# Kernel optimization log

Hardware: AMD Instinct MI355X
Metric: run time of the kernel (lower is better)

Reference implementation:

```python
import jax, jax.numpy as jnp
import numpy as np

K_PERIODS = 4
PMAX = 64
MIN_PERIOD = 8


def setup_inputs() -> dict:
    key = jax.random.key(0)
    x = jax.random.normal(key, (32, 512, 64), dtype=jnp.float32)  # [B, T, N]
    return {"x": x}


def reference(x):
    """Dense, fixed-shape equivalent of PeriodicityTransform.forward (mask=None).

    Instead of a Python list of variable-shape PeriodGroup tiles, returns a
    padded tensor values[bn, k, c, p] where for each (sequence bn, freq rank k)
    with period P and cycles C, values[bn, k, :C, :P] equals the torch tile
    seqs[bn, T-C*P : T].reshape(C, P); entries outside (C, P) are zero.
    Also returns the integer periods and cycles per (bn, k).
    """
    B, T, N = x.shape
    BN = B * N
    seqs = jnp.transpose(x, (0, 2, 1)).reshape(BN, T)  # [BN, T]

    # top-k nonzero FFT frequencies (DC bin zeroed out)
    spec = jnp.fft.rfft(seqs, axis=-1)
    mag2 = spec.real ** 2 + spec.imag ** 2
    mag2 = mag2.at[..., 0].set(0.0)
    _, kidx = jax.lax.top_k(mag2, K_PERIODS)  # [BN, K]
    kidx = jnp.maximum(kidx, 1)

    # periods = clamp(T // f, min=MIN_PERIOD, max=PMAX); cycles = T // period
    periods = jnp.clip(T // kidx, MIN_PERIOD, PMAX)  # [BN, K]
    cycles = T // periods                              # [BN, K]

    cmax = T // MIN_PERIOD  # static upper bound on cycles
    i = jnp.arange(cmax)[:, None]   # cycle index  [Cmax, 1]
    j = jnp.arange(PMAX)[None, :]   # phase index  [1, Pmax]

    start = T - cycles * periods                                   # [BN, K]
    idx = start[..., None, None] + i * periods[..., None, None] + j  # [BN,K,Cmax,Pmax]
    idx = jnp.clip(idx, 0, T - 1)
    valid = (i < cycles[..., None, None]) & (j < periods[..., None, None])

    gathered = jnp.take_along_axis(
        seqs[:, None, :], idx.reshape(BN, K_PERIODS, -1), axis=-1
    ).reshape(BN, K_PERIODS, cmax, PMAX)
    values = jnp.where(valid, gathered, jnp.float32(0.0))
    return values, periods, cycles
```

## Files before the change

### kernel.cpp

```cpp
#include <hip/hip_runtime.h>
#include <math.h>

#define TT 512
#define KP 4

typedef unsigned long long u64;

#define SYNCL() asm volatile("s_waitcnt lgkmcnt(0)\n\ts_barrier" ::: "memory")

__global__ __launch_bounds__(256) void periodicity_kernel(const float* __restrict__ x,
                                                          float* __restrict__ out) {
    const int bn   = blockIdx.x;
    const int tid  = threadIdx.x;
    const int lane = tid & 63;
    const int wid  = tid >> 6;
    const int b = bn >> 6;
    const int n = bn & 63;

    __shared__ float2 tw[TT];
    __shared__ __align__(16) float row[TT];
    __shared__ float2 buf[TT];
    __shared__ u64    keys[256];
    __shared__ int    fin8[8];
    __shared__ float  candMagF[8];
    __shared__ double candV8[8];
    __shared__ unsigned char w4tab[64];

    float sv, cv;
    sincosf((float)(2.0 * M_PI / 512.0) * (float)tid, &sv, &cv);
    tw[tid]       = make_float2(cv, -sv);
    tw[tid + 256] = make_float2(-cv, sv);
    if (tid < 64) {
        int W = 512 / (tid + 1);
        W = W < 8 ? 8 : (W > 64 ? 64 : W);
        w4tab[tid] = (unsigned char)((W + 3) >> 2);
    }

    const float* xb = x + (size_t)b * (TT * 64) + n;
    {
        float v0 = xb[(size_t)tid * 64];
        float v1 = xb[(size_t)(tid + 256) * 64];
        row[tid] = v0;  row[tid + 256] = v1;
        float sum = v0 + v1, dif = v0 - v1;
        buf[tid]       = make_float2(sum, 0.f);
        buf[tid + 256] = make_float2(dif * cv, -dif * sv);
    }
    SYNCL();

    float* outv = out + (size_t)bn * (KP * 64 * 64);
    {
        const int j  = tid & 15;
        const int cb = tid >> 4;
        #pragma unroll
        for (int iter = 0; iter < 4; ++iter) {
            const int c = 8 + iter * 16 + cb;
            if (c < 64 && j >= (int)w4tab[c]) {
                const float4 z = make_float4(0.f, 0.f, 0.f, 0.f);
                #pragma unroll
                for (int k = 0; k < KP; ++k)
                    *(float4*)(outv + k * 4096 + c * 64 + j * 4) = z;
            }
        }
    }

    #pragma unroll
    for (int stg = 0; stg < 4; ++stg) {
        if (tid < 128) {
            const int Q  = 64 >> (2 * stg);
            const int B4 = Q << 2;
            const int h  = tid >> 6;
            const int fj = tid & 63;
            const int g  = fj >> (6 - 2 * stg);
            const int i  = fj & (Q - 1);
            float2* bb = &buf[h << 8];
            const int base = g * B4 + i;
            float2 x0 = bb[base],         x1 = bb[base + Q];
            float2 x2 = bb[base + 2 * Q], x3 = bb[base + 3 * Q];
            float2 A  = make_float2(x0.x + x2.x, x0.y + x2.y);
            float2 Bm = make_float2(x0.x - x2.x, x0.y - x2.y);
            float2 Cc = make_float2(x1.x + x3.x, x1.y + x3.y);
            float2 D  = make_float2(x1.x - x3.x, x1.y - x3.y);
            float2 y0 = make_float2(A.x + Cc.x, A.y + Cc.y);
            float2 y2 = make_float2(A.x - Cc.x, A.y - Cc.y);
            float2 y1 = make_float2(Bm.x + D.y, Bm.y - D.x);
            float2 y3 = make_float2(Bm.x - D.y, Bm.y + D.x);
            const int m = i << (1 + 2 * stg);
            float2 t1 = tw[m], t2 = tw[2 * m], t3 = tw[3 * m];
            bb[base]         = y0;
            bb[base + Q]     = make_float2(y1.x * t1.x - y1.y * t1.y, y1.x * t1.y + y1.y * t1.x);
            bb[base + 2 * Q] = make_float2(y2.x * t2.x - y2.y * t2.y, y2.x * t2.y + y2.y * t2.x);
            bb[base + 3 * Q] = make_float2(y3.x * t3.x - y3.y * t3.y, y3.x * t3.y + y3.y * t3.x);
        }
        SYNCL();
    }

    #pragma unroll
    for (int hh = 0; hh < 2; ++hh) {
        const int p = tid;
        const int kp = ((p & 3) << 6) | (((p >> 2) & 3) << 4) | (((p >> 4) & 3) << 2) | ((p >> 6) & 3);
        const int f = 2 * kp + hh;
        if (f >= 1 && f <= 256) {
            float2 v = buf[hh * 256 + p];
            float mag = v.x * v.x + v.y * v.y;
            keys[f - 1] = ((u64)__float_as_uint(mag) << 32) | (u64)(255 - (f - 1));
        }
    }
    SYNCL();

    if (wid == 0) {
        u64 k0 = keys[lane * 4 + 0];
        u64 k1 = keys[lane * 4 + 1];
        u64 k2 = keys[lane * 4 + 2];
        u64 k3 = keys[lane * 4 + 3];
        #define CSWAP(a, b) { if (a < b) { u64 _t = a; a = b; b = _t; } }
        CSWAP(k0, k1) CSWAP(k2, k3) CSWAP(k0, k2) CSWAP(k1, k3) CSWAP(k1, k2)
        #undef CSWAP
        #pragma unroll
        for (int r = 0; r < 8; ++r) {
            u64 w = k0;
            #pragma unroll
            for (int off = 32; off >= 1; off >>= 1) {
                u64 o = __shfl_xor(w, off);
                if (o > w) w = o;
            }
            if (k0 == w) { k0 = k1; k1 = k2; k2 = k3; k3 = 0; }
            if (lane == 0) {
                fin8[r] = 256 - (int)(w & 0xff);
                candMagF[r] = __uint_as_float((unsigned)(w >> 32));
            }
        }
    }
    SYNCL();

    int per[KP], cycv[KP], stv[KP];
    {
        const float m0 = candMagF[0], m1 = candMagF[1], m2 = candMagF[2],
                    m3 = candMagF[3], m4 = candMagF[4];
        const bool needRefine = ((m0 - m1) <= 1e-4f * m0) || ((m1 - m2) <= 1e-4f * m1) ||
                                ((m2 - m3) <= 1e-4f * m2) || ((m3 - m4) <= 1e-4f * m3);
        int bins[KP];
        if (!needRefine) {
            #pragma unroll
            for (int k = 0; k < KP; ++k) bins[k] = fin8[k];
        } else {
            {
                const int cid = tid >> 5;
                const int sub = tid & 31;
                const int fc  = fin8[cid];
                const int t0  = sub * 16;
                const double W = 6.2831853071795864769 / 512.0;
                double zr, zi, wr, wi;
                sincos(W * (double)((fc * t0) & 511), &zi, &zr);
                sincos(W * (double)fc, &wi, &wr);
                double ar = 0.0, ai = 0.0;
                const float4* r4 = (const float4*)row;
                #pragma unroll
                for (int v4i = 0; v4i < 4; ++v4i) {
                    float4 xv = r4[sub * 4 + v4i];
                    #define STEP(comp)                                   \
                        { double xd = (double)xv.comp;                   \
                          ar = fma(xd, zr, ar); ai = fma(xd, zi, ai);    \
                          double tq = zr * wr - zi * wi;                 \
                          zi = fma(zr, wi, zi * wr); zr = tq; }
                    STEP(x) STEP(y) STEP(z) STEP(w)
                    #undef STEP
                }
                #pragma unroll
                for (int off = 16; off >= 1; off >>= 1) {
                    ar += __shfl_xor(ar, off);
                    ai += __shfl_xor(ai, off);
                }
                if (sub == 0) candV8[cid] = ar * ar + ai * ai;
            }
            SYNCL();
            unsigned chosen = 0;
            #pragma unroll
            for (int k = 0; k < KP; ++k) {
                double bv = -1.0; int bbin = 0x7fffffff; int bj = 0;
                #pragma unroll
                for (int j = 0; j < 8; ++j) {
                    if (chosen & (1u << j)) continue;
                    double vj = candV8[j];
                    int    bjn = fin8[j];
                    if (vj > bv || (vj == bv && bjn < bbin)) { bv = vj; bbin = bjn; bj = j; }
                }
                chosen |= (1u << bj);
                bins[k] = bbin;
            }
        }
        #pragma unroll
        for (int k = 0; k < KP; ++k) {
            int p = TT / bins[k];
            p = p < 8 ? 8 : (p > 64 ? 64 : p);
            per[k]  = p;
            cycv[k] = TT / p;
            stv[k]  = TT - cycv[k] * p;
        }
    }

    const size_t VOFF = (size_t)2048 * KP * 64 * 64;
    if (tid == 0) {
        #pragma unroll
        for (int k = 0; k < KP; ++k) {
            out[VOFF + (size_t)bn * KP + k]        = (float)per[k];
            out[VOFF + 8192 + (size_t)bn * KP + k] = (float)cycv[k];
        }
    }

    {
        const int c  = tid >> 2;
        const int j0 = tid & 3;
        const int W4c = (int)w4tab[c];
        #pragma unroll
        for (int k = 0; k < KP; ++k) {
            const int P = per[k], C = cycv[k], S0 = stv[k];
            const int inC  = (c < C) ? 1 : 0;
            const int base = S0 + c * P;
            #pragma unroll
            for (int m = 0; m < 4; ++m) {
                const int j = j0 + (m << 2);
                if (j < W4c) {
                    const int p0 = j << 2;
                    float4 v = make_float4(0.f, 0.f, 0.f, 0.f);
                    if (inC) {
                        if (p0     < P) v.x = row[base + p0];
                        if (p0 + 1 < P) v.y = row[base + p0 + 1];
                        if (p0 + 2 < P) v.z = row[base + p0 + 2];
                        if (p0 + 3 < P) v.w = row[base + p0 + 3];
                    }
                    *(float4*)(outv + k * 4096 + c * 64 + p0) = v;
                }
            }
        }
    }
}

extern "C" void kernel_launch(void* const* d_in, const int* in_sizes, int n_in,
                              void* d_out, int out_size, void* d_ws, size_t ws_size,
                              hipStream_t stream) {
    const float* x = (const float*)d_in[0];
    float* out = (float*)d_out;
    hipLaunchKernelGGL(periodicity_kernel, dim3(2048), dim3(256), 0, stream, x, out);
}
```

Baseline: 35.75 us.

## Process four sequences per block with warp-specialized FFT and store waves

Each block now handles four sequences: four waves each run a full radix-4 FFT, top-k selection and optional refinement for one sequence without block barriers, while four other waves zero-fill the padding and then write the gathered tiles once periods are published through shared memory. This removes most block-wide barriers from the FFT and sort stages and overlaps the zero-fill stores with the compute. It costs more shared memory per block and gives each FFT wave more serial work, since only 64 lanes now do each FFT. The grid shrinks to 512 blocks of 512 threads.

```diff
diff --git a/kernel.cpp b/kernel.cpp
--- a/kernel.cpp
+++ b/kernel.cpp
@@ -8,155 +8,147 @@
 
 #define SYNCL() asm volatile("s_waitcnt lgkmcnt(0)\n\ts_barrier" ::: "memory")
 
-__global__ __launch_bounds__(256) void periodicity_kernel(const float* __restrict__ x,
-                                                          float* __restrict__ out) {
-    const int bn   = blockIdx.x;
+__global__ __launch_bounds__(512, 4) void periodicity_kernel(const float* __restrict__ x,
+                                                             float* __restrict__ out) {
+    const int blk  = blockIdx.x;
     const int tid  = threadIdx.x;
     const int lane = tid & 63;
     const int wid  = tid >> 6;
-    const int b = bn >> 6;
-    const int n = bn & 63;
 
     __shared__ float2 tw[TT];
-    __shared__ __align__(16) float row[TT];
-    __shared__ float2 buf[TT];
-    __shared__ u64    keys[256];
-    __shared__ int    fin8[8];
-    __shared__ float  candMagF[8];
-    __shared__ double candV8[8];
-    __shared__ unsigned char w4tab[64];
-
-    float sv, cv;
-    sincosf((float)(2.0 * M_PI / 512.0) * (float)tid, &sv, &cv);
-    tw[tid]       = make_float2(cv, -sv);
-    tw[tid + 256] = make_float2(-cv, sv);
-    if (tid < 64) {
-        int W = 512 / (tid + 1);
-        W = W < 8 ? 8 : (W > 64 ? 64 : W);
-        w4tab[tid] = (unsigned char)((W + 3) >> 2);
+    __shared__ __align__(16) float rowl[4][TT];
+    __shared__ float2 buf[4][TT];
+    __shared__ u64    keys[4][256];
+    __shared__ int    fin8s[4][8];
+    __shared__ double candV8[4][8];
+    __shared__ int    pstore[4][12];
+
+    const size_t VOFF = (size_t)2048 * KP * 64 * 64;
+
+    float v[8];
+    if (wid < 4) {
+        const int bn = blk * 4 + wid;
+        const int b = bn >> 6, n = bn & 63;
+        const float* xb = x + (size_t)b * (TT * 64) + n;
+        #pragma unroll
+        for (int q = 0; q < 8; ++q) v[q] = xb[(size_t)(lane + 64 * q) * 64];
     }
 
-    const float* xb = x + (size_t)b * (TT * 64) + n;
     {
-        float v0 = xb[(size_t)tid * 64];
-        float v1 = xb[(size_t)(tid + 256) * 64];
-        row[tid] = v0;  row[tid + 256] = v1;
-        float sum = v0 + v1, dif = v0 - v1;
-        buf[tid]       = make_float2(sum, 0.f);
-        buf[tid + 256] = make_float2(dif * cv, -dif * sv);
+        float s, c;
+        sincosf((float)(2.0 * M_PI / 512.0) * (float)tid, &s, &c);
+        tw[tid] = make_float2(c, -s);
     }
     SYNCL();
 
-    float* outv = out + (size_t)bn * (KP * 64 * 64);
-    {
-        const int j  = tid & 15;
-        const int cb = tid >> 4;
-        #pragma unroll
-        for (int iter = 0; iter < 4; ++iter) {
-            const int c = 8 + iter * 16 + cb;
-            if (c < 64 && j >= (int)w4tab[c]) {
-                const float4 z = make_float4(0.f, 0.f, 0.f, 0.f);
-                #pragma unroll
-                for (int k = 0; k < KP; ++k)
-                    *(float4*)(outv + k * 4096 + c * 64 + j * 4) = z;
-            }
-        }
-    }
-
-    #pragma unroll
-    for (int stg = 0; stg < 4; ++stg) {
-        if (tid < 128) {
-            const int Q  = 64 >> (2 * stg);
-            const int B4 = Q << 2;
-            const int h  = tid >> 6;
-            const int fj = tid & 63;
-            const int g  = fj >> (6 - 2 * stg);
-            const int i  = fj & (Q - 1);
-            float2* bb = &buf[h << 8];
-            const int base = g * B4 + i;
-            float2 x0 = bb[base],         x1 = bb[base + Q];
-            float2 x2 = bb[base + 2 * Q], x3 = bb[base + 3 * Q];
-            float2 A  = make_float2(x0.x + x2.x, x0.y + x2.y);
-            float2 Bm = make_float2(x0.x - x2.x, x0.y - x2.y);
-            float2 Cc = make_float2(x1.x + x3.x, x1.y + x3.y);
-            float2 D  = make_float2(x1.x - x3.x, x1.y - x3.y);
-            float2 y0 = make_float2(A.x + Cc.x, A.y + Cc.y);
-            float2 y2 = make_float2(A.x - Cc.x, A.y - Cc.y);
-            float2 y1 = make_float2(Bm.x + D.y, Bm.y - D.x);
-            float2 y3 = make_float2(Bm.x - D.y, Bm.y + D.x);
-            const int m = i << (1 + 2 * stg);
-            float2 t1 = tw[m], t2 = tw[2 * m], t3 = tw[3 * m];
-            bb[base]         = y0;
-            bb[base + Q]     = make_float2(y1.x * t1.x - y1.y * t1.y, y1.x * t1.y + y1.y * t1.x);
-            bb[base + 2 * Q] = make_float2(y2.x * t2.x - y2.y * t2.y, y2.x * t2.y + y2.y * t2.x);
-            bb[base + 3 * Q] = make_float2(y3.x * t3.x - y3.y * t3.y, y3.x * t3.y + y3.y * t3.x);
-        }
-        SYNCL();
-    }
-
-    #pragma unroll
-    for (int hh = 0; hh < 2; ++hh) {
-        const int p = tid;
-        const int kp = ((p & 3) << 6) | (((p >> 2) & 3) << 4) | (((p >> 4) & 3) << 2) | ((p >> 6) & 3);
-        const int f = 2 * kp + hh;
-        if (f >= 1 && f <= 256) {
-            float2 v = buf[hh * 256 + p];
-            float mag = v.x * v.x + v.y * v.y;
-            keys[f - 1] = ((u64)__float_as_uint(mag) << 32) | (u64)(255 - (f - 1));
-        }
-    }
-    SYNCL();
-
-    if (wid == 0) {
-        u64 k0 = keys[lane * 4 + 0];
-        u64 k1 = keys[lane * 4 + 1];
-        u64 k2 = keys[lane * 4 + 2];
-        u64 k3 = keys[lane * 4 + 3];
-        #define CSWAP(a, b) { if (a < b) { u64 _t = a; a = b; b = _t; } }
-        CSWAP(k0, k1) CSWAP(k2, k3) CSWAP(k0, k2) CSWAP(k1, k3) CSWAP(k1, k2)
-        #undef CSWAP
-        #pragma unroll
-        for (int r = 0; r < 8; ++r) {
-            u64 w = k0;
-            #pragma unroll
-            for (int off = 32; off >= 1; off >>= 1) {
-                u64 o = __shfl_xor(w, off);
-                if (o > w) w = o;
-            }
-            if (k0 == w) { k0 = k1; k1 = k2; k2 = k3; k3 = 0; }
-            if (lane == 0) {
-                fin8[r] = 256 - (int)(w & 0xff);
-                candMagF[r] = __uint_as_float((unsigned)(w >> 32));
-            }
-        }
-    }
-    SYNCL();
-
-    int per[KP], cycv[KP], stv[KP];
-    {
-        const float m0 = candMagF[0], m1 = candMagF[1], m2 = candMagF[2],
-                    m3 = candMagF[3], m4 = candMagF[4];
-        const bool needRefine = ((m0 - m1) <= 1e-4f * m0) || ((m1 - m2) <= 1e-4f * m1) ||
-                                ((m2 - m3) <= 1e-4f * m2) || ((m3 - m4) <= 1e-4f * m3);
+    if (wid < 4) {
+        const int r  = wid;
+        const int bn = blk * 4 + r;
+
+        #pragma unroll
+        for (int q = 0; q < 8; ++q) rowl[r][lane + 64 * q] = v[q];
+        #pragma unroll
+        for (int q = 0; q < 4; ++q) {
+            const int t = lane + 64 * q;
+            float sum = v[q] + v[q + 4], dif = v[q] - v[q + 4];
+            float2 w = tw[t];
+            buf[r][t]       = make_float2(sum, 0.f);
+            buf[r][t + 256] = make_float2(dif * w.x, dif * w.y);
+        }
+
+        #pragma unroll
+        for (int stg = 0; stg < 4; ++stg) {
+            #pragma unroll
+            for (int h = 0; h < 2; ++h) {
+                const int Q  = 64 >> (2 * stg);
+                const int B4 = Q << 2;
+                const int g  = lane >> (6 - 2 * stg);
+                const int i  = lane & (Q - 1);
+                float2* bb = &buf[r][h << 8];
+                const int base = g * B4 + i;
+                float2 x0 = bb[base],         x1 = bb[base + Q];
+                float2 x2 = bb[base + 2 * Q], x3 = bb[base + 3 * Q];
+                float2 A  = make_float2(x0.x + x2.x, x0.y + x2.y);
+                float2 Bm = make_float2(x0.x - x2.x, x0.y - x2.y);
+                float2 Cc = make_float2(x1.x + x3.x, x1.y + x3.y);
+                float2 D  = make_float2(x1.x - x3.x, x1.y - x3.y);
+                float2 y0 = make_float2(A.x + Cc.x, A.y + Cc.y);
+                float2 y2 = make_float2(A.x - Cc.x, A.y - Cc.y);
+                float2 y1 = make_float2(Bm.x + D.y, Bm.y - D.x);
+                float2 y3 = make_float2(Bm.x - D.y, Bm.y + D.x);
+                const int m = i << (1 + 2 * stg);
+                float2 t1 = tw[m], t2 = tw[2 * m], t3 = tw[3 * m];
+                bb[base]         = y0;
+                bb[base + Q]     = make_float2(y1.x * t1.x - y1.y * t1.y, y1.x * t1.y + y1.y * t1.x);
+                bb[base + 2 * Q] = make_float2(y2.x * t2.x - y2.y * t2.y, y2.x * t2.y + y2.y * t2.x);
+                bb[base + 3 * Q] = make_float2(y3.x * t3.x - y3.y * t3.y, y3.x * t3.y + y3.y * t3.x);
+            }
+        }
+
+        #pragma unroll
+        for (int q = 0; q < 8; ++q) {
+            const int pos = lane + 64 * q;
+            const int p = pos & 255, h = pos >> 8;
+            const int kp = ((p & 3) << 6) | (((p >> 2) & 3) << 4) | (((p >> 4) & 3) << 2) | ((p >> 6) & 3);
+            const int f = 2 * kp + h;
+            if (f >= 1 && f <= 256) {
+                float2 vv = buf[r][pos];
+                float mag = vv.x * vv.x + vv.y * vv.y;
+                keys[r][f - 1] = ((u64)__float_as_uint(mag) << 32) | (u64)(255 - (f - 1));
+            }
+        }
+
+        int   fbin[8];
+        float cmag[8];
+        {
+            u64 k0 = keys[r][lane * 4 + 0];
+            u64 k1 = keys[r][lane * 4 + 1];
+            u64 k2 = keys[r][lane * 4 + 2];
+            u64 k3 = keys[r][lane * 4 + 3];
+            #define CSWAP(a, b) { if (a < b) { u64 _t = a; a = b; b = _t; } }
+            CSWAP(k0, k1) CSWAP(k2, k3) CSWAP(k0, k2) CSWAP(k1, k3) CSWAP(k1, k2)
+            #undef CSWAP
+            #pragma unroll
+            for (int rr = 0; rr < 8; ++rr) {
+                u64 w = k0;
+                #pragma unroll
+                for (int off = 32; off >= 1; off >>= 1) {
+                    u64 o = __shfl_xor(w, off);
+                    if (o > w) w = o;
+                }
+                if (k0 == w) { k0 = k1; k1 = k2; k2 = k3; k3 = 0; }
+                fbin[rr] = 256 - (int)(w & 0xff);
+                cmag[rr] = __uint_as_float((unsigned)(w >> 32));
+            }
+        }
+        if (lane == 0) {
+            #pragma unroll
+            for (int rr = 0; rr < 8; ++rr) fin8s[r][rr] = fbin[rr];
+        }
+
+        const bool needRefine =
+            ((cmag[0] - cmag[1]) <= 1e-4f * cmag[0]) || ((cmag[1] - cmag[2]) <= 1e-4f * cmag[1]) ||
+            ((cmag[2] - cmag[3]) <= 1e-4f * cmag[2]) || ((cmag[3] - cmag[4]) <= 1e-4f * cmag[3]);
+
         int bins[KP];
         if (!needRefine) {
             #pragma unroll
-            for (int k = 0; k < KP; ++k) bins[k] = fin8[k];
+            for (int k = 0; k < KP; ++k) bins[k] = fbin[k];
         } else {
             {
-                const int cid = tid >> 5;
-                const int sub = tid & 31;
-                const int fc  = fin8[cid];
-                const int t0  = sub * 16;
+                const int cid = lane >> 3;
+                const int sub = lane & 7;
+                const int fc  = fin8s[r][cid];
+                const int t0  = sub * 64;
                 const double W = 6.2831853071795864769 / 512.0;
                 double zr, zi, wr, wi;
                 sincos(W * (double)((fc * t0) & 511), &zi, &zr);
                 sincos(W * (double)fc, &wi, &wr);
                 double ar = 0.0, ai = 0.0;
-                const float4* r4 = (const float4*)row;
-                #pragma unroll
-                for (int v4i = 0; v4i < 4; ++v4i) {
-                    float4 xv = r4[sub * 4 + v4i];
+                const float4* r4 = (const float4*)rowl[r];
+                #pragma unroll
+                for (int v4i = 0; v4i < 16; ++v4i) {
+                    float4 xv = r4[sub * 16 + v4i];
                     #define STEP(comp)                                   \
                         { double xd = (double)xv.comp;                   \
                           ar = fma(xd, zr, ar); ai = fma(xd, zi, ai);    \
@@ -166,13 +158,12 @@
                     #undef STEP
                 }
                 #pragma unroll
-                for (int off = 16; off >= 1; off >>= 1) {
+                for (int off = 4; off >= 1; off >>= 1) {
                     ar += __shfl_xor(ar, off);
                     ai += __shfl_xor(ai, off);
                 }
-                if (sub == 0) candV8[cid] = ar * ar + ai * ai;
-            }
-            SYNCL();
+                if (sub == 0) candV8[r][cid] = ar * ar + ai * ai;
+            }
             unsigned chosen = 0;
             #pragma unroll
             for (int k = 0; k < KP; ++k) {
@@ -180,14 +171,16 @@
                 #pragma unroll
                 for (int j = 0; j < 8; ++j) {
                     if (chosen & (1u << j)) continue;
-                    double vj = candV8[j];
-                    int    bjn = fin8[j];
+                    double vj = candV8[r][j];
+                    int    bjn = fbin[j];
                     if (vj > bv || (vj == bv && bjn < bbin)) { bv = vj; bbin = bjn; bj = j; }
                 }
                 chosen |= (1u << bj);
                 bins[k] = bbin;
             }
         }
+
+        int per[KP], cycv[KP], stv[KP];
         #pragma unroll
         for (int k = 0; k < KP; ++k) {
             int p = TT / bins[k];
@@ -196,39 +189,72 @@
             cycv[k] = TT / p;
             stv[k]  = TT - cycv[k] * p;
         }
-    }
-
-    const size_t VOFF = (size_t)2048 * KP * 64 * 64;
-    if (tid == 0) {
+        if (lane == 0) {
+            #pragma unroll
+            for (int k = 0; k < KP; ++k) {
+                pstore[r][k]     = per[k];
+                pstore[r][4 + k] = cycv[k];
+                pstore[r][8 + k] = stv[k];
+                out[VOFF + (size_t)bn * KP + k]        = (float)per[k];
+                out[VOFF + 8192 + (size_t)bn * KP + k] = (float)cycv[k];
+            }
+        }
+        SYNCL();
+    } else {
+        const int r  = wid - 4;
+        const int bn = blk * 4 + r;
+        float* outv = out + (size_t)bn * (KP * 64 * 64);
+        const int cr = lane >> 4;
+        const int j  = lane & 15;
+        const float4 z = make_float4(0.f, 0.f, 0.f, 0.f);
+
+        #pragma unroll
+        for (int c0 = 8; c0 < 64; c0 += 4) {
+            const int c = c0 + cr;
+            int W = 512 / (c + 1);
+            W = W < 8 ? 8 : W;
+            const int W4c = (W + 3) >> 2;
+            if (j >= W4c) {
+                #pragma unroll
+                for (int k = 0; k < KP; ++k)
+                    *(float4*)(outv + k * 4096 + c * 64 + j * 4) = z;
+            }
+        }
+        SYNCL();
+
+        int P[KP], C[KP], S0[KP];
         #pragma unroll
         for (int k = 0; k < KP; ++k) {
-            out[VOFF + (size_t)bn * KP + k]        = (float)per[k];
-            out[VOFF + 8192 + (size_t)bn * KP + k] = (float)cycv[k];
-        }
-    }
-
-    {
-        const int c  = tid >> 2;
-        const int j0 = tid & 3;
-        const int W4c = (int)w4tab[c];
-        #pragma unroll
-        for (int k = 0; k < KP; ++k) {
-            const int P = per[k], C = cycv[k], S0 = stv[k];
-            const int inC  = (c < C) ? 1 : 0;
-            const int base = S0 + c * P;
-            #pragma unroll
-            for (int m = 0; m < 4; ++m) {
-                const int j = j0 + (m << 2);
-                if (j < W4c) {
-                    const int p0 = j << 2;
-                    float4 v = make_float4(0.f, 0.f, 0.f, 0.f);
-                    if (inC) {
-                        if (p0     < P) v.x = row[base + p0];
-                        if (p0 + 1 < P) v.y = row[base + p0 + 1];
-                        if (p0 + 2 < P) v.z = row[base + p0 + 2];
-                        if (p0 + 3 < P) v.w = row[base + p0 + 3];
+            P[k]  = pstore[r][k];
+            C[k]  = pstore[r][4 + k];
+            S0[k] = pstore[r][8 + k];
+        }
+        #pragma unroll
+        for (int c0 = 0; c0 < 64; c0 += 4) {
+            const int c = c0 + cr;
+            int W = 512 / (c + 1);
+            W = W < 8 ? 8 : (W > 64 ? 64 : W);
+            const int W4c = (W + 3) >> 2;
+            if (j < W4c) {
+                const int p0 = j << 2;
+                #pragma unroll
+                for (int k = 0; k < KP; ++k) {
+                    float4 vv = z;
+                    if (c < C[k]) {
+                        const int base = S0[k] + c * P[k] + p0;
+                        if (p0 + 3 < P[k]) {
+                            vv.x = rowl[r][base];
+                            vv.y = rowl[r][base + 1];
+                            vv.z = rowl[r][base + 2];
+                            vv.w = rowl[r][base + 3];
+                        } else {
+                            if (p0     < P[k]) vv.x = rowl[r][base];
+                            if (p0 + 1 < P[k]) vv.y = rowl[r][base + 1];
+                            if (p0 + 2 < P[k]) vv.z = rowl[r][base + 2];
+                            if (p0 + 3 < P[k]) vv.w = rowl[r][base + 3];
+                        }
                     }
-                    *(float4*)(outv + k * 4096 + c * 64 + p0) = v;
+                    *(float4*)(outv + k * 4096 + c * 64 + p0) = vv;
                 }
             }
         }
@@ -240,5 +266,5 @@
                               hipStream_t stream) {
     const float* x = (const float*)d_in[0];
     float* out = (float*)d_out;
-    hipLaunchKernelGGL(periodicity_kernel, dim3(2048), dim3(256), 0, stream, x, out);
+    hipLaunchKernelGGL(periodicity_kernel, dim3(512), dim3(512), 0, stream, x, out);
 }
```

Result: slower. 39.17 us (+9.6%).

## Fuse last FFT stage into magnitude pass and unify coalesced output writes

Applied to the files above, without the earlier changes.

The final radix-4 FFT stage is folded into the magnitude/key-building pass, which removes one shared-memory round trip and one barrier. The early zero-fill phase and the w4tab lookup table go away. All output tiles are now written in one loop where each thread stores contiguous float4 values across full rows, so every block writes its whole 64KB output region in fully coalesced order. This may write more zeros than before but drops the scattered partial-row writes and the extra setup work.

```diff
diff --git a/kernel.cpp b/kernel.cpp
--- a/kernel.cpp
+++ b/kernel.cpp
@@ -24,17 +24,11 @@
     __shared__ int    fin8[8];
     __shared__ float  candMagF[8];
     __shared__ double candV8[8];
-    __shared__ unsigned char w4tab[64];
 
     float sv, cv;
     sincosf((float)(2.0 * M_PI / 512.0) * (float)tid, &sv, &cv);
     tw[tid]       = make_float2(cv, -sv);
     tw[tid + 256] = make_float2(-cv, sv);
-    if (tid < 64) {
-        int W = 512 / (tid + 1);
-        W = W < 8 ? 8 : (W > 64 ? 64 : W);
-        w4tab[tid] = (unsigned char)((W + 3) >> 2);
-    }
 
     const float* xb = x + (size_t)b * (TT * 64) + n;
     {
@@ -47,24 +41,8 @@
     }
     SYNCL();
 
-    float* outv = out + (size_t)bn * (KP * 64 * 64);
-    {
-        const int j  = tid & 15;
-        const int cb = tid >> 4;
-        #pragma unroll
-        for (int iter = 0; iter < 4; ++iter) {
-            const int c = 8 + iter * 16 + cb;
-            if (c < 64 && j >= (int)w4tab[c]) {
-                const float4 z = make_float4(0.f, 0.f, 0.f, 0.f);
-                #pragma unroll
-                for (int k = 0; k < KP; ++k)
-                    *(float4*)(outv + k * 4096 + c * 64 + j * 4) = z;
-            }
-        }
-    }
-
     #pragma unroll
-    for (int stg = 0; stg < 4; ++stg) {
+    for (int stg = 0; stg < 3; ++stg) {
         if (tid < 128) {
             const int Q  = 64 >> (2 * stg);
             const int B4 = Q << 2;
@@ -94,15 +72,33 @@
         SYNCL();
     }
 
-    #pragma unroll
-    for (int hh = 0; hh < 2; ++hh) {
-        const int p = tid;
-        const int kp = ((p & 3) << 6) | (((p >> 2) & 3) << 4) | (((p >> 4) & 3) << 2) | ((p >> 6) & 3);
-        const int f = 2 * kp + hh;
-        if (f >= 1 && f <= 256) {
-            float2 v = buf[hh * 256 + p];
-            float mag = v.x * v.x + v.y * v.y;
-            keys[f - 1] = ((u64)__float_as_uint(mag) << 32) | (u64)(255 - (f - 1));
+    if (tid < 128) {
+        const int h = tid >> 6;
+        const int g = tid & 63;
+        float2* bb = &buf[h << 8];
+        const int base = g << 2;
+        float2 x0 = bb[base],     x1 = bb[base + 1];
+        float2 x2 = bb[base + 2], x3 = bb[base + 3];
+        float2 A  = make_float2(x0.x + x2.x, x0.y + x2.y);
+        float2 Bm = make_float2(x0.x - x2.x, x0.y - x2.y);
+        float2 Cc = make_float2(x1.x + x3.x, x1.y + x3.y);
+        float2 D  = make_float2(x1.x - x3.x, x1.y - x3.y);
+        float2 y0 = make_float2(A.x + Cc.x, A.y + Cc.y);
+        float2 y2 = make_float2(A.x - Cc.x, A.y - Cc.y);
+        float2 y1 = make_float2(Bm.x + D.y, Bm.y - D.x);
+        float2 y3 = make_float2(Bm.x - D.y, Bm.y + D.x);
+        const int revg = ((g & 3) << 4) | (((g >> 2) & 3) << 2) | ((g >> 4) & 3);
+        const int f0 = 2 * revg + h;
+        float mags[4];
+        mags[0] = y0.x * y0.x + y0.y * y0.y;
+        mags[1] = y1.x * y1.x + y1.y * y1.y;
+        mags[2] = y2.x * y2.x + y2.y * y2.y;
+        mags[3] = y3.x * y3.x + y3.y * y3.y;
+        #pragma unroll
+        for (int j = 0; j < 4; ++j) {
+            const int f = f0 + 128 * j;
+            if (f >= 1 && f <= 256)
+                keys[f - 1] = ((u64)__float_as_uint(mags[j]) << 32) | (u64)(255 - (f - 1));
         }
     }
     SYNCL();
@@ -207,31 +203,30 @@
         }
     }
 
-    {
-        const int c  = tid >> 2;
-        const int j0 = tid & 3;
-        const int W4c = (int)w4tab[c];
-        #pragma unroll
-        for (int k = 0; k < KP; ++k) {
-            const int P = per[k], C = cycv[k], S0 = stv[k];
-            const int inC  = (c < C) ? 1 : 0;
+    float* outv = out + (size_t)bn * (KP * 64 * 64);
+    const int c_local = tid >> 4;
+    const int p0 = (tid & 15) << 2;
+    #pragma unroll
+    for (int it = 0; it < 16; ++it) {
+        const int k = it >> 2;
+        const int c = ((it & 3) << 4) + c_local;
+        float4 v = make_float4(0.f, 0.f, 0.f, 0.f);
+        const int P = per[k], C = cycv[k], S0 = stv[k];
+        if (c < C) {
             const int base = S0 + c * P;
-            #pragma unroll
-            for (int m = 0; m < 4; ++m) {
-                const int j = j0 + (m << 2);
-                if (j < W4c) {
-                    const int p0 = j << 2;
-                    float4 v = make_float4(0.f, 0.f, 0.f, 0.f);
-                    if (inC) {
-                        if (p0     < P) v.x = row[base + p0];
-                        if (p0 + 1 < P) v.y = row[base + p0 + 1];
-                        if (p0 + 2 < P) v.z = row[base + p0 + 2];
-                        if (p0 + 3 < P) v.w = row[base + p0 + 3];
-                    }
-                    *(float4*)(outv + k * 4096 + c * 64 + p0) = v;
-                }
-            }
-        }
+            if (p0 + 3 < P) {
+                v.x = row[base + p0];
+                v.y = row[base + p0 + 1];
+                v.z = row[base + p0 + 2];
+                v.w = row[base + p0 + 3];
+            } else {
+                if (p0     < P) v.x = row[base + p0];
+                if (p0 + 1 < P) v.y = row[base + p0 + 1];
+                if (p0 + 2 < P) v.z = row[base + p0 + 2];
+                if (p0 + 3 < P) v.w = row[base + p0 + 3];
+            }
+        }
+        *(float4*)(outv + (size_t)it * 1024 + (size_t)tid * 4) = v;
     }
 }
 
```

Result: faster. 30.47 us (-14.8%).
